# Kernel tuning notes

Measured on AMD Instinct MI355X. Metric: run time of the kernel, lower is better.

Reference implementation:

```python
import jax, jax.numpy as jnp
import numpy as np

DIM = 1024
HEADS = 16
D_HEAD = 64
INNER = HEADS * D_HEAD  # 1024
CTX_DIM = 768
FF_INNER = 4 * DIM  # 4096
EPS = 1e-5
SCALE = D_HEAD ** -0.5


def _layer_norm(x, g, b):
    m = jnp.mean(x, axis=-1, keepdims=True)
    v = jnp.mean(jnp.square(x - m), axis=-1, keepdims=True)
    return (x - m) * jax.lax.rsqrt(v + EPS) * g + b


def _attention(x, ctx, wq, wk, wv, wo, bo):
    B, S, _ = x.shape
    T = ctx.shape[1]
    # project and split heads -> [B, H, S, Dh]
    q = (x @ wq).reshape(B, S, HEADS, D_HEAD).transpose(0, 2, 1, 3)
    k = (ctx @ wk).reshape(B, T, HEADS, D_HEAD).transpose(0, 2, 1, 3)
    v = (ctx @ wv).reshape(B, T, HEADS, D_HEAD).transpose(0, 2, 1, 3)
    attn = jnp.einsum('bhid,bhjd->bhij', q, k) * SCALE
    attn = jax.nn.softmax(attn, axis=-1)
    out = jnp.einsum('bhij,bhjd->bhid', attn, v)  # [B, H, S, Dh]
    out = out.transpose(0, 2, 1, 3).reshape(B, S, INNER)
    return out @ wo + bo


def setup_inputs() -> dict:
    key = jax.random.key(0)
    ks = jax.random.split(key, 20)
    rn = lambda k, shape, s=0.02: jax.random.normal(k, shape, dtype=jnp.float32) * s
    inp = {
        'hidden_states': jax.random.normal(ks[0], (4, 2048, DIM), dtype=jnp.float32),
        'context': jax.random.normal(ks[1], (4, 77, CTX_DIM), dtype=jnp.float32),
        # self-attention
        'wq1': rn(ks[2], (DIM, INNER)), 'wk1': rn(ks[3], (DIM, INNER)),
        'wv1': rn(ks[4], (DIM, INNER)),
        'wo1': rn(ks[5], (INNER, DIM)), 'bo1': jnp.zeros((DIM,), jnp.float32),
        # cross-attention (k/v from context dim 768)
        'wq2': rn(ks[6], (DIM, INNER)), 'wk2': rn(ks[7], (CTX_DIM, INNER)),
        'wv2': rn(ks[8], (CTX_DIM, INNER)),
        'wo2': rn(ks[9], (INNER, DIM)), 'bo2': jnp.zeros((DIM,), jnp.float32),
        # GEGLU feed-forward
        'w_ff1': rn(ks[10], (DIM, 2 * FF_INNER)), 'b_ff1': jnp.zeros((2 * FF_INNER,), jnp.float32),
        'w_ff2': rn(ks[11], (FF_INNER, DIM)), 'b_ff2': jnp.zeros((DIM,), jnp.float32),
        # layer norms
        'ln1_g': jnp.ones((DIM,), jnp.float32), 'ln1_b': jnp.zeros((DIM,), jnp.float32),
        'ln2_g': jnp.ones((DIM,), jnp.float32), 'ln2_b': jnp.zeros((DIM,), jnp.float32),
        'ln3_g': jnp.ones((DIM,), jnp.float32), 'ln3_b': jnp.zeros((DIM,), jnp.float32),
    }
    return inp


def reference(hidden_states, context, wq1, wk1, wv1, wo1, bo1,
              wq2, wk2, wv2, wo2, bo2, w_ff1, b_ff1, w_ff2, b_ff2,
              ln1_g, ln1_b, ln2_g, ln2_b, ln3_g, ln3_b):
    # self-attention, pre-norm residual
    h = hidden_states
    h = h + _attention(_layer_norm(h, ln1_g, ln1_b), _layer_norm(h, ln1_g, ln1_b),
                       wq1, wk1, wv1, wo1, bo1)
    # cross-attention
    h = h + _attention(_layer_norm(h, ln2_g, ln2_b), context,
                       wq2, wk2, wv2, wo2, bo2)
    # GEGLU feed-forward
    x = _layer_norm(h, ln3_g, ln3_b) @ w_ff1 + b_ff1
    lin, gate = jnp.split(x, 2, axis=2)
    h = h + (lin * jax.nn.gelu(gate)) @ w_ff2 + b_ff2
    return h
```

## Files before the change

### kernel.cpp

```cpp
#include <hip/hip_runtime.h>

#define DIMM 1024
#define NHEADS 16
#define DHEAD 64
#define BATCH 4
#define SEQ 2048
#define TCTX 77
#define CTXD 768
#define FFI 4096

typedef float f32x4 __attribute__((ext_vector_type(4)));
typedef __bf16 bf16x8 __attribute__((ext_vector_type(8)));

__device__ __forceinline__ float bf2f(unsigned short u){
  union { unsigned int i; float f; } c; c.i = ((unsigned int)u) << 16; return c.f;
}
__device__ __forceinline__ unsigned short f2bf(float f){
  union { float f; unsigned int i; } c; c.f = f;
  unsigned int i = c.i;
  return (unsigned short)((i + 0x7fffu + ((i >> 16) & 1u)) >> 16);
}
__device__ __forceinline__ void cp16(const unsigned short* g, unsigned short* l){
  __builtin_amdgcn_global_load_lds(
      (const __attribute__((address_space(1))) unsigned int*)g,
      (__attribute__((address_space(3))) unsigned int*)l, 16, 0, 0);
}

__global__ __launch_bounds__(256) void ln_kernel(const float* __restrict__ x,
                                                 const float* __restrict__ g,
                                                 const float* __restrict__ bb,
                                                 unsigned short* __restrict__ y)
{
  int row = blockIdx.x, tid = threadIdx.x;
  float4 raw = ((const float4*)(x + (size_t)row * DIMM))[tid];
  float v0 = raw.x, v1 = raw.y, v2 = raw.z, v3 = raw.w;
  float s  = v0 + v1 + v2 + v3;
  float sq = v0*v0 + v1*v1 + v2*v2 + v3*v3;
  #pragma unroll
  for (int off = 32; off; off >>= 1){ s += __shfl_xor(s, off); sq += __shfl_xor(sq, off); }
  __shared__ float sm[8];
  int wave = tid >> 6, lane = tid & 63;
  if (lane == 0){ sm[wave] = s; sm[4 + wave] = sq; }
  __syncthreads();
  s  = sm[0] + sm[1] + sm[2] + sm[3];
  sq = sm[4] + sm[5] + sm[6] + sm[7];
  float mean = s * (1.f / DIMM);
  float var  = sq * (1.f / DIMM) - mean * mean;
  float rstd = rsqrtf(var + 1e-5f);
  float4 gr = ((const float4*)g)[tid];
  float4 br = ((const float4*)bb)[tid];
  ushort4 o;
  o.x = f2bf((v0 - mean) * rstd * gr.x + br.x);
  o.y = f2bf((v1 - mean) * rstd * gr.y + br.y);
  o.z = f2bf((v2 - mean) * rstd * gr.z + br.z);
  o.w = f2bf((v3 - mean) * rstd * gr.w + br.w);
  ((ushort4*)(y + (size_t)row * DIMM))[tid] = o;
}

__global__ __launch_bounds__(256) void wt_kernel(const float* __restrict__ in,
                                                 unsigned short* __restrict__ out,
                                                 int K, int N)
{
  __shared__ float t[32][33];
  int tx = threadIdx.x & 31, ty = threadIdx.x >> 5;
  int k0 = blockIdx.y * 32, n0 = blockIdx.x * 32;
  #pragma unroll
  for (int i = 0; i < 4; i++)
    t[ty + i * 8][tx] = in[(size_t)(k0 + ty + i * 8) * N + n0 + tx];
  __syncthreads();
  #pragma unroll
  for (int i = 0; i < 4; i++)
    out[(size_t)(n0 + ty + i * 8) * K + k0 + tx] = f2bf(t[tx][ty + i * 8]);
}

#define CTXE (TCTX * BATCH * CTXD)
__global__ __launch_bounds__(256) void ctxcvt_kernel(const float* __restrict__ in,
                                                     unsigned short* __restrict__ out)
{
  int e = (blockIdx.x * 256 + threadIdx.x) * 4;
  float4 v;
  if (e < CTXE) v = *(const float4*)(in + e);
  else { v.x = 0.f; v.y = 0.f; v.z = 0.f; v.w = 0.f; }
  ushort4 o; o.x = f2bf(v.x); o.y = f2bf(v.y); o.z = f2bf(v.z); o.w = f2bf(v.w);
  *(ushort4*)(out + e) = o;
}

template<int RESF, int CF32>
__global__ __launch_bounds__(256) void gemm_bt(
    const unsigned short* __restrict__ A, int lda,
    const unsigned short* __restrict__ Bt, int ldb,
    const float* __restrict__ bias, const void* __restrict__ resv,
    void* __restrict__ Cv, int ldc,
    int M, int N, int K)
{
  __shared__ __align__(16) unsigned short As[128][64];
  __shared__ __align__(16) unsigned short Bs[128][64];
  int tid = threadIdx.x;
  int n0 = blockIdx.x * 128, row0 = blockIdx.y * 128;
  int wave = tid >> 6, lane = tid & 63, quad = lane >> 4, l16 = lane & 15;
  int wm = (wave >> 1) * 64, wn = (wave & 1) * 64;
  int wrow = wave * 32;
  int lrow = lane >> 3, lgrp = lane & 7;
  int gcol = ((lgrp ^ lrow) * 8);

  f32x4 acc[4][4];
  #pragma unroll
  for (int mt = 0; mt < 4; mt++)
    #pragma unroll
    for (int nt = 0; nt < 4; nt++) acc[mt][nt] = 0.f;

  for (int k0 = 0; k0 < K; k0 += 64) {
    const unsigned short* ga = A  + (size_t)(row0 + wrow + lrow) * lda + k0 + gcol;
    const unsigned short* gb = Bt + (size_t)(n0  + wrow + lrow) * ldb + k0 + gcol;
    #pragma unroll
    for (int i = 0; i < 4; i++){
      cp16(ga + (size_t)(8 * i) * lda, &As[wrow + 8 * i][0]);
      cp16(gb + (size_t)(8 * i) * ldb, &Bs[wrow + 8 * i][0]);
    }
    __syncthreads();
    #pragma unroll
    for (int kc = 0; kc < 2; kc++){
      bf16x8 af[4], bf[4];
      #pragma unroll
      for (int mt = 0; mt < 4; mt++){
        int R = wm + mt * 16 + l16;
        af[mt] = *(const bf16x8*)&As[R][((kc * 4 + quad) ^ (R & 7)) * 8];
      }
      #pragma unroll
      for (int nt = 0; nt < 4; nt++){
        int R = wn + nt * 16 + l16;
        bf[nt] = *(const bf16x8*)&Bs[R][((kc * 4 + quad) ^ (R & 7)) * 8];
      }
      #pragma unroll
      for (int mt = 0; mt < 4; mt++)
        #pragma unroll
        for (int nt = 0; nt < 4; nt++)
          acc[mt][nt] = __builtin_amdgcn_mfma_f32_16x16x32_bf16(af[mt], bf[nt], acc[mt][nt], 0, 0, 0);
    }
    __syncthreads();
  }

  #pragma unroll
  for (int nt = 0; nt < 4; nt++){
    int c = n0 + wn + nt * 16 + l16;
    float bv = bias ? bias[c] : 0.f;
    #pragma unroll
    for (int mt = 0; mt < 4; mt++){
      int rbase = row0 + wm + mt * 16 + quad * 4;
      #pragma unroll
      for (int rr = 0; rr < 4; rr++){
        int r = rbase + rr;
        if (r < M) {
          float val = acc[mt][nt][rr] + bv;
          size_t idx = (size_t)r * ldc + c;
          if (RESF) val += ((const float*)resv)[idx];
          if (CF32) ((float*)Cv)[idx] = val;
          else      ((unsigned short*)Cv)[idx] = f2bf(val);
        }
      }
    }
  }
}

__global__ __launch_bounds__(256) void ff1_geglu_bt(
    const unsigned short* __restrict__ A,
    const unsigned short* __restrict__ BtW,
    const float* __restrict__ bias,
    unsigned short* __restrict__ Z, int M)
{
  __shared__ __align__(16) unsigned short As[128][64];
  __shared__ __align__(16) unsigned short BsL[128][64];
  __shared__ __align__(16) unsigned short BsG[128][64];
  int tid = threadIdx.x;
  int n0 = blockIdx.x * 128, row0 = blockIdx.y * 128;
  int wave = tid >> 6, lane = tid & 63, quad = lane >> 4, l16 = lane & 15;
  int wm = (wave >> 1) * 64, wn = (wave & 1) * 64;
  int wrow = wave * 32;
  int lrow = lane >> 3, lgrp = lane & 7;
  int gcol = ((lgrp ^ lrow) * 8);

  f32x4 accL[4][4], accG[4][4];
  #pragma unroll
  for (int mt = 0; mt < 4; mt++)
    #pragma unroll
    for (int nt = 0; nt < 4; nt++){ accL[mt][nt] = 0.f; accG[mt][nt] = 0.f; }

  for (int k0 = 0; k0 < DIMM; k0 += 64) {
    const unsigned short* ga = A   + (size_t)(row0 + wrow + lrow) * DIMM + k0 + gcol;
    const unsigned short* gl = BtW + (size_t)(n0  + wrow + lrow) * DIMM + k0 + gcol;
    const unsigned short* gg = BtW + (size_t)(FFI + n0 + wrow + lrow) * DIMM + k0 + gcol;
    #pragma unroll
    for (int i = 0; i < 4; i++){
      cp16(ga + (size_t)(8 * i) * DIMM, &As[wrow + 8 * i][0]);
      cp16(gl + (size_t)(8 * i) * DIMM, &BsL[wrow + 8 * i][0]);
      cp16(gg + (size_t)(8 * i) * DIMM, &BsG[wrow + 8 * i][0]);
    }
    __syncthreads();
    #pragma unroll
    for (int kc = 0; kc < 2; kc++){
      bf16x8 af[4], b[4];
      #pragma unroll
      for (int mt = 0; mt < 4; mt++){
        int R = wm + mt * 16 + l16;
        af[mt] = *(const bf16x8*)&As[R][((kc * 4 + quad) ^ (R & 7)) * 8];
      }
      #pragma unroll
      for (int nt = 0; nt < 4; nt++){
        int R = wn + nt * 16 + l16;
        b[nt] = *(const bf16x8*)&BsL[R][((kc * 4 + quad) ^ (R & 7)) * 8];
      }
      #pragma unroll
      for (int mt = 0; mt < 4; mt++)
        #pragma unroll
        for (int nt = 0; nt < 4; nt++)
          accL[mt][nt] = __builtin_amdgcn_mfma_f32_16x16x32_bf16(af[mt], b[nt], accL[mt][nt], 0, 0, 0);
      #pragma unroll
      for (int nt = 0; nt < 4; nt++){
        int R = wn + nt * 16 + l16;
        b[nt] = *(const bf16x8*)&BsG[R][((kc * 4 + quad) ^ (R & 7)) * 8];
      }
      #pragma unroll
      for (int mt = 0; mt < 4; mt++)
        #pragma unroll
        for (int nt = 0; nt < 4; nt++)
          accG[mt][nt] = __builtin_amdgcn_mfma_f32_16x16x32_bf16(af[mt], b[nt], accG[mt][nt], 0, 0, 0);
    }
    __syncthreads();
  }

  #pragma unroll
  for (int nt = 0; nt < 4; nt++){
    int c = n0 + wn + nt * 16 + l16;
    float bvL = bias[c];
    float bvG = bias[c + FFI];
    #pragma unroll
    for (int mt = 0; mt < 4; mt++){
      int rbase = row0 + wm + mt * 16 + quad * 4;
      #pragma unroll
      for (int rr = 0; rr < 4; rr++){
        float lin = accL[mt][nt][rr] + bvL;
        float g   = accG[mt][nt][rr] + bvG;
        float y = 0.7978845608028654f * (g + 0.044715f * g * g * g);
        float e = __builtin_amdgcn_exp2f(y * 2.8853900817779268f);
        float t = 1.f - 2.f * __builtin_amdgcn_rcpf(e + 1.f);
        Z[(size_t)(rbase + rr) * FFI + c] = f2bf(lin * 0.5f * g * (1.f + t));
      }
    }
  }
}

__global__ __launch_bounds__(512, 8) void attn_mfma(
    const unsigned short* __restrict__ Q, int ldq,
    const unsigned short* __restrict__ Kb,
    const unsigned short* __restrict__ Vb, int ldkv,
    unsigned short* __restrict__ O,
    int S, int T, float scale)
{
  int tid = threadIdx.x, wave = tid >> 6, lane = tid & 63;
  int quad = lane >> 4, l16 = lane & 15;
  int bh = blockIdx.y, b = bh >> 4, h = bh & 15;
  int qw = blockIdx.x * 128 + wave * 16;

  __shared__ __align__(16) unsigned short Ks[64][64];
  __shared__ __align__(16) unsigned short Vp[64][64];

  float qs = scale * 1.44269504088896f;
  bf16x8 Qf[2];
  #pragma unroll
  for (int kc = 0; kc < 2; kc++){
    const unsigned short* qp = Q + ((size_t)b * S + qw + l16) * ldq
                                 + h * DHEAD + kc * 32 + quad * 8;
    union { float4 v; unsigned short u[8]; } ld; ld.v = *(const float4*)qp;
    union { bf16x8 v; unsigned short u[8]; } sc;
    #pragma unroll
    for (int j = 0; j < 8; j++) sc.u[j] = f2bf(bf2f(ld.u[j]) * qs);
    Qf[kc] = sc.v;
  }

  f32x4 Oacc[4];
  float lp = 0.f;
  #pragma unroll
  for (int nt = 0; nt < 4; nt++) Oacc[nt] = 0.f;

  int lrow = lane >> 3, lgrp = lane & 7;
  int gcol = (lgrp ^ lrow) * 8;
  int vj = lane;
  int vchunk = ((vj >> 5) << 2) | ((vj >> 2) & 3);
  int velem  = (((vj >> 4) & 1) << 2) | (vj & 3);
  int dbs = wave * 8;

  for (int j0 = 0; j0 < T; j0 += 64){
    bool tail = (j0 + 64 > T);
    if (!tail){
      const unsigned short* gk = Kb + ((size_t)b * T + j0 + wave * 8 + lrow) * ldkv
                                    + h * DHEAD + gcol;
      cp16(gk, &Ks[wave * 8][0]);
    } else {
      int key = tid >> 3, g = tid & 7;
      float4 kv;
      if (j0 + key < T) kv = *(const float4*)(Kb + ((size_t)b * T + j0 + key) * ldkv + h * DHEAD + g * 8);
      else { kv.x = 0.f; kv.y = 0.f; kv.z = 0.f; kv.w = 0.f; }
      *(float4*)&Ks[key][(g ^ (key & 7)) * 8] = kv;
    }
    {
      union { float4 v; unsigned short u[8]; } vv;
      if (j0 + vj < T) vv.v = *(const float4*)(Vb + ((size_t)b * T + j0 + vj) * ldkv + h * DHEAD + dbs);
      else { vv.v.x = 0.f; vv.v.y = 0.f; vv.v.z = 0.f; vv.v.w = 0.f; }
      #pragma unroll
      for (int u = 0; u < 8; u++)
        Vp[dbs + u][((vchunk ^ u) << 3) | velem] = vv.u[u];
    }
    __syncthreads();

    union pfu { bf16x8 v; __bf16 e[8]; } pf[2];
    {
      f32x4 sT[4];
      #pragma unroll
      for (int nt = 0; nt < 4; nt++){
        sT[nt] = 0.f;
        #pragma unroll
        for (int kc = 0; kc < 2; kc++){
          bf16x8 kf = *(const bf16x8*)&Ks[nt * 16 + l16][((kc * 4 + quad) ^ (l16 & 7)) * 8];
          sT[nt] = __builtin_amdgcn_mfma_f32_16x16x32_bf16(kf, Qf[kc], sT[nt], 0, 0, 0);
        }
      }
      #pragma unroll
      for (int nt = 0; nt < 4; nt++)
        #pragma unroll
        for (int rr = 0; rr < 4; rr++){
          float sv = sT[nt][rr];
          if (tail && (j0 + nt * 16 + quad * 4 + rr) >= T) sv = -1e30f;
          float p = __builtin_amdgcn_exp2f(fminf(sv, 108.f));
          lp += p;
          pf[nt >> 1].e[(nt & 1) * 4 + rr] = (__bf16)p;
        }
    }

    #pragma unroll
    for (int kc = 0; kc < 2; kc++)
      #pragma unroll
      for (int nt = 0; nt < 4; nt++){
        int R = nt * 16 + l16;
        bf16x8 vf = *(const bf16x8*)&Vp[R][((kc * 4 + quad) ^ (R & 7)) * 8];
        Oacc[nt] = __builtin_amdgcn_mfma_f32_16x16x32_bf16(pf[kc].v, vf, Oacc[nt], 0, 0, 0);
      }
    __syncthreads();
  }

  float l = lp;
  l += __shfl_xor(l, 16);
  l += __shfl_xor(l, 32);
  float inv[4];
  #pragma unroll
  for (int rr = 0; rr < 4; rr++)
    inv[rr] = 1.f / __shfl(l, quad * 4 + rr);
  #pragma unroll
  for (int nt = 0; nt < 4; nt++)
    #pragma unroll
    for (int rr = 0; rr < 4; rr++){
      size_t idx = ((size_t)b * S + qw + quad * 4 + rr) * DIMM
                   + h * DHEAD + nt * 16 + l16;
      O[idx] = f2bf(Oacc[nt][rr] * inv[rr]);
    }
}

extern "C" void kernel_launch(void* const* d_in, const int* in_sizes, int n_in,
                              void* d_out, int out_size, void* d_ws, size_t ws_size,
                              hipStream_t stream)
{
  const float* h0   = (const float*)d_in[0];
  const float* ctx  = (const float*)d_in[1];
  const float* wq1  = (const float*)d_in[2];
  const float* wk1  = (const float*)d_in[3];
  const float* wv1  = (const float*)d_in[4];
  const float* wo1  = (const float*)d_in[5];
  const float* bo1  = (const float*)d_in[6];
  const float* wq2  = (const float*)d_in[7];
  const float* wk2  = (const float*)d_in[8];
  const float* wv2  = (const float*)d_in[9];
  const float* wo2  = (const float*)d_in[10];
  const float* bo2  = (const float*)d_in[11];
  const float* wff1 = (const float*)d_in[12];
  const float* bff1 = (const float*)d_in[13];
  const float* wff2 = (const float*)d_in[14];
  const float* bff2 = (const float*)d_in[15];
  const float* ln1g = (const float*)d_in[16];
  const float* ln1b = (const float*)d_in[17];
  const float* ln2g = (const float*)d_in[18];
  const float* ln2b = (const float*)d_in[19];
  const float* ln3g = (const float*)d_in[20];
  const float* ln3b = (const float*)d_in[21];

  unsigned short* wsp = (unsigned short*)d_ws;
  const size_t RD = (size_t)BATCH * SEQ * DIMM;
  unsigned short* xn  = wsp;
  unsigned short* qkv = wsp + RD;
  unsigned short* ar  = wsp + 4 * RD;
  unsigned short* zb  = qkv;
  float* hres = (float*)d_out;

  const size_t M1 = (size_t)1024 * 1024;
  const int ROWS = BATCH * SEQ;
  const int CROWS = BATCH * TCTX;
  const float scale = 0.125f;
  dim3 blk(256);
  dim3 ablk(512);
  dim3 attn_grid(SEQ / 128, BATCH * NHEADS);

  wt_kernel<<<dim3(32, 32), blk, 0, stream>>>(wq1, ar,          DIMM, DIMM);
  wt_kernel<<<dim3(32, 32), blk, 0, stream>>>(wk1, ar + M1,     DIMM, DIMM);
  wt_kernel<<<dim3(32, 32), blk, 0, stream>>>(wv1, ar + 2 * M1, DIMM, DIMM);
  wt_kernel<<<dim3(32, 32), blk, 0, stream>>>(wo1, ar + 3 * M1, DIMM, DIMM);
  ln_kernel<<<ROWS, blk, 0, stream>>>(h0, ln1g, ln1b, xn);
  gemm_bt<0,0><<<dim3(3072 / 128, ROWS / 128), blk, 0, stream>>>(
      xn, DIMM, ar, DIMM, nullptr, nullptr, qkv, 3072, ROWS, 3072, DIMM);
  attn_mfma<<<attn_grid, ablk, 0, stream>>>(qkv, 3072, qkv + 1024, qkv + 2048, 3072, xn, SEQ, SEQ, scale);
  gemm_bt<1,1><<<dim3(DIMM / 128, ROWS / 128), blk, 0, stream>>>(
      xn, DIMM, ar + 3 * M1, DIMM, bo1, h0, hres, DIMM, ROWS, DIMM, DIMM);

  unsigned short* wq2T  = ar;
  unsigned short* wkv2T = ar + M1;
  unsigned short* wo2T  = ar + M1 + (size_t)2048 * CTXD;
  unsigned short* xc    = wo2T + M1;
  wt_kernel<<<dim3(32, 32), blk, 0, stream>>>(wq2, wq2T, DIMM, DIMM);
  wt_kernel<<<dim3(32, 24), blk, 0, stream>>>(wk2, wkv2T, CTXD, DIMM);
  wt_kernel<<<dim3(32, 24), blk, 0, stream>>>(wv2, wkv2T + (size_t)1024 * CTXD, CTXD, DIMM);
  wt_kernel<<<dim3(32, 32), blk, 0, stream>>>(wo2, wo2T, DIMM, DIMM);
  ctxcvt_kernel<<<(384 * CTXD / 4) / 256, blk, 0, stream>>>(ctx, xc);
  ln_kernel<<<ROWS, blk, 0, stream>>>(hres, ln2g, ln2b, xn);
  gemm_bt<0,0><<<dim3(DIMM / 128, ROWS / 128), blk, 0, stream>>>(
      xn, DIMM, wq2T, DIMM, nullptr, nullptr, qkv, DIMM, ROWS, DIMM, DIMM);
  unsigned short* kvc = qkv + RD;
  gemm_bt<0,0><<<dim3(2048 / 128, 3), blk, 0, stream>>>(
      xc, CTXD, wkv2T, CTXD, nullptr, nullptr, kvc, 2048, CROWS, 2048, CTXD);
  attn_mfma<<<attn_grid, ablk, 0, stream>>>(qkv, 1024, kvc, kvc + 1024, 2048, xn, SEQ, TCTX, scale);
  gemm_bt<1,1><<<dim3(DIMM / 128, ROWS / 128), blk, 0, stream>>>(
      xn, DIMM, wo2T, DIMM, bo2, hres, hres, DIMM, ROWS, DIMM, DIMM);

  unsigned short* wff1T = ar;
  unsigned short* wff2T = ar + 8 * M1;
  wt_kernel<<<dim3(256, 32),  blk, 0, stream>>>(wff1, wff1T, DIMM, 2 * FFI);
  wt_kernel<<<dim3(32, 128),  blk, 0, stream>>>(wff2, wff2T, FFI, DIMM);
  ln_kernel<<<ROWS, blk, 0, stream>>>(hres, ln3g, ln3b, xn);
  for (int half = 0; half < 2; half++){
    int r0 = half * 4096;
    ff1_geglu_bt<<<dim3(FFI / 128, 4096 / 128), blk, 0, stream>>>(
        xn + (size_t)r0 * DIMM, wff1T, bff1, zb, 4096);
    gemm_bt<1,1><<<dim3(DIMM / 128, 4096 / 128), blk, 0, stream>>>(
        zb, FFI, wff2T, FFI, bff2, hres + (size_t)r0 * DIMM,
        hres + (size_t)r0 * DIMM, DIMM, 4096, DIMM, FFI);
  }
}
```

Before: 1.032 ms.

## Process two query tiles per wave in attention to reuse K/V loads

Each wave in the attention kernel now handles 32 query rows as two 16-row MFMA tiles instead of one. Every K/V tile staged in shared memory and every V fragment read therefore feeds twice the MFMA work. The grid is halved to match, and launch bounds drop to 4 blocks per SM to allow more registers. The cost is higher register pressure and fewer blocks, which lowers occupancy and parallelism for the self and cross attention calls.

After: 994.8 us. 1.04x faster.

```diff
diff --git a/kernel.cpp b/kernel.cpp
--- a/kernel.cpp
+++ b/kernel.cpp
@@ -249,7 +249,7 @@
   }
 }
 
-__global__ __launch_bounds__(512, 8) void attn_mfma(
+__global__ __launch_bounds__(512, 4) void attn_mfma(
     const unsigned short* __restrict__ Q, int ldq,
     const unsigned short* __restrict__ Kb,
     const unsigned short* __restrict__ Vb, int ldkv,
@@ -259,28 +259,32 @@
   int tid = threadIdx.x, wave = tid >> 6, lane = tid & 63;
   int quad = lane >> 4, l16 = lane & 15;
   int bh = blockIdx.y, b = bh >> 4, h = bh & 15;
-  int qw = blockIdx.x * 128 + wave * 16;
+  int qw = blockIdx.x * 256 + wave * 32;
 
   __shared__ __align__(16) unsigned short Ks[64][64];
   __shared__ __align__(16) unsigned short Vp[64][64];
 
   float qs = scale * 1.44269504088896f;
-  bf16x8 Qf[2];
-  #pragma unroll
-  for (int kc = 0; kc < 2; kc++){
-    const unsigned short* qp = Q + ((size_t)b * S + qw + l16) * ldq
-                                 + h * DHEAD + kc * 32 + quad * 8;
-    union { float4 v; unsigned short u[8]; } ld; ld.v = *(const float4*)qp;
-    union { bf16x8 v; unsigned short u[8]; } sc;
-    #pragma unroll
-    for (int j = 0; j < 8; j++) sc.u[j] = f2bf(bf2f(ld.u[j]) * qs);
-    Qf[kc] = sc.v;
-  }
-
-  f32x4 Oacc[4];
-  float lp = 0.f;
-  #pragma unroll
-  for (int nt = 0; nt < 4; nt++) Oacc[nt] = 0.f;
+  bf16x8 Qf[2][2];
+  #pragma unroll
+  for (int mt = 0; mt < 2; mt++)
+    #pragma unroll
+    for (int kc = 0; kc < 2; kc++){
+      const unsigned short* qp = Q + ((size_t)b * S + qw + mt * 16 + l16) * ldq
+                                   + h * DHEAD + kc * 32 + quad * 8;
+      union { float4 v; unsigned short u[8]; } ld; ld.v = *(const float4*)qp;
+      union { bf16x8 v; unsigned short u[8]; } sc;
+      #pragma unroll
+      for (int j = 0; j < 8; j++) sc.u[j] = f2bf(bf2f(ld.u[j]) * qs);
+      Qf[mt][kc] = sc.v;
+    }
+
+  f32x4 Oacc[2][4];
+  float lp[2] = {0.f, 0.f};
+  #pragma unroll
+  for (int mt = 0; mt < 2; mt++)
+    #pragma unroll
+    for (int nt = 0; nt < 4; nt++) Oacc[mt][nt] = 0.f;
 
   int lrow = lane >> 3, lgrp = lane & 7;
   int gcol = (lgrp ^ lrow) * 8;
@@ -312,8 +316,9 @@
     }
     __syncthreads();
 
-    union pfu { bf16x8 v; __bf16 e[8]; } pf[2];
-    {
+    union pfu { bf16x8 v; __bf16 e[8]; } pf[2][2];
+    #pragma unroll
+    for (int mt = 0; mt < 2; mt++){
       f32x4 sT[4];
       #pragma unroll
       for (int nt = 0; nt < 4; nt++){
@@ -321,7 +326,7 @@
         #pragma unroll
         for (int kc = 0; kc < 2; kc++){
           bf16x8 kf = *(const bf16x8*)&Ks[nt * 16 + l16][((kc * 4 + quad) ^ (l16 & 7)) * 8];
-          sT[nt] = __builtin_amdgcn_mfma_f32_16x16x32_bf16(kf, Qf[kc], sT[nt], 0, 0, 0);
+          sT[nt] = __builtin_amdgcn_mfma_f32_16x16x32_bf16(kf, Qf[mt][kc], sT[nt], 0, 0, 0);
         }
       }
       #pragma unroll
@@ -331,8 +336,8 @@
           float sv = sT[nt][rr];
           if (tail && (j0 + nt * 16 + quad * 4 + rr) >= T) sv = -1e30f;
           float p = __builtin_amdgcn_exp2f(fminf(sv, 108.f));
-          lp += p;
-          pf[nt >> 1].e[(nt & 1) * 4 + rr] = (__bf16)p;
+          lp[mt] += p;
+          pf[mt][nt >> 1].e[(nt & 1) * 4 + rr] = (__bf16)p;
         }
     }
 
@@ -342,26 +347,31 @@
       for (int nt = 0; nt < 4; nt++){
         int R = nt * 16 + l16;
         bf16x8 vf = *(const bf16x8*)&Vp[R][((kc * 4 + quad) ^ (R & 7)) * 8];
-        Oacc[nt] = __builtin_amdgcn_mfma_f32_16x16x32_bf16(pf[kc].v, vf, Oacc[nt], 0, 0, 0);
-      }
-    __syncthreads();
-  }
-
-  float l = lp;
-  l += __shfl_xor(l, 16);
-  l += __shfl_xor(l, 32);
-  float inv[4];
-  #pragma unroll
-  for (int rr = 0; rr < 4; rr++)
-    inv[rr] = 1.f / __shfl(l, quad * 4 + rr);
-  #pragma unroll
-  for (int nt = 0; nt < 4; nt++)
-    #pragma unroll
-    for (int rr = 0; rr < 4; rr++){
-      size_t idx = ((size_t)b * S + qw + quad * 4 + rr) * DIMM
-                   + h * DHEAD + nt * 16 + l16;
-      O[idx] = f2bf(Oacc[nt][rr] * inv[rr]);
-    }
+        #pragma unroll
+        for (int mt = 0; mt < 2; mt++)
+          Oacc[mt][nt] = __builtin_amdgcn_mfma_f32_16x16x32_bf16(pf[mt][kc].v, vf, Oacc[mt][nt], 0, 0, 0);
+      }
+    __syncthreads();
+  }
+
+  #pragma unroll
+  for (int mt = 0; mt < 2; mt++){
+    float l = lp[mt];
+    l += __shfl_xor(l, 16);
+    l += __shfl_xor(l, 32);
+    float inv[4];
+    #pragma unroll
+    for (int rr = 0; rr < 4; rr++)
+      inv[rr] = 1.f / __shfl(l, quad * 4 + rr);
+    #pragma unroll
+    for (int nt = 0; nt < 4; nt++)
+      #pragma unroll
+      for (int rr = 0; rr < 4; rr++){
+        size_t idx = ((size_t)b * S + qw + mt * 16 + quad * 4 + rr) * DIMM
+                     + h * DHEAD + nt * 16 + l16;
+        O[idx] = f2bf(Oacc[mt][nt][rr] * inv[rr]);
+      }
+  }
 }
 
 extern "C" void kernel_launch(void* const* d_in, const int* in_sizes, int n_in,
@@ -405,7 +415,7 @@
   const float scale = 0.125f;
   dim3 blk(256);
   dim3 ablk(512);
-  dim3 attn_grid(SEQ / 128, BATCH * NHEADS);
+  dim3 attn_grid(SEQ / 256, BATCH * NHEADS);
 
   wt_kernel<<<dim3(32, 32), blk, 0, stream>>>(wq1, ar,          DIMM, DIMM);
   wt_kernel<<<dim3(32, 32), blk, 0, stream>>>(wk1, ar + M1,     DIMM, DIMM);
```
